# Optimization experiments

Hardware: AMD Instinct MI355X
Metric: run time of the kernel (lower is better)

## Reference

```python
import jax, jax.numpy as jnp
import numpy as np

N = 50000        # nodes
E = 800000       # random edges (self loops appended inside reference, per PyG default)
IN = 128         # in_channels
H1, C1 = 8, 64   # conv1: heads, hidden_channels
NUM_CLASSES = 2  # conv2 out (heads=1, concat=False)
NEG_SLOPE = 0.2  # PyG GATConv default LeakyReLU slope


def setup_inputs() -> dict:
    key = jax.random.key(0)
    ks = jax.random.split(key, 12)
    x = jax.random.normal(ks[0], (N, IN), dtype=jnp.float32)
    edge_index = jax.random.randint(ks[1], (2, E), 0, N)
    # conv1 params: W1 [IN, H1*C1], att vectors [H1, C1], bias [H1*C1]
    W1 = jax.random.normal(ks[2], (IN, H1 * C1), dtype=jnp.float32) / np.sqrt(IN)
    a_src1 = jax.random.normal(ks[3], (H1, C1), dtype=jnp.float32) / np.sqrt(C1)
    a_dst1 = jax.random.normal(ks[4], (H1, C1), dtype=jnp.float32) / np.sqrt(C1)
    b1 = jnp.zeros((H1 * C1,), dtype=jnp.float32)
    # conv2 params: heads=1, out=NUM_CLASSES
    W2 = jax.random.normal(ks[5], (H1 * C1, 1 * NUM_CLASSES), dtype=jnp.float32) / np.sqrt(H1 * C1)
    a_src2 = jax.random.normal(ks[6], (1, NUM_CLASSES), dtype=jnp.float32) / np.sqrt(NUM_CLASSES)
    a_dst2 = jax.random.normal(ks[7], (1, NUM_CLASSES), dtype=jnp.float32) / np.sqrt(NUM_CLASSES)
    b2 = jnp.zeros((NUM_CLASSES,), dtype=jnp.float32)
    return {"x": x, "edge_index": edge_index, "W1": W1, "a_src1": a_src1,
            "a_dst1": a_dst1, "b1": b1, "W2": W2, "a_src2": a_src2,
            "a_dst2": a_dst2, "b2": b2}


def gat_layer(x, src, dst, W, a_src, a_dst, bias, concat):
    n = x.shape[0]
    heads, ch = a_src.shape
    h = (x @ W).reshape(n, heads, ch)                      # [N,H,C]
    alpha_s = jnp.einsum('nhc,hc->nh', h, a_src)           # per-node src score
    alpha_d = jnp.einsum('nhc,hc->nh', h, a_dst)           # per-node dst score
    e = jax.nn.leaky_relu(alpha_s[src] + alpha_d[dst], NEG_SLOPE)  # [Etot,H]
    # segment softmax over edges grouped by destination node
    m = jax.ops.segment_max(e, dst, num_segments=n)
    ex = jnp.exp(e - m[dst])
    den = jax.ops.segment_sum(ex, dst, num_segments=n)
    alpha = ex / den[dst]                                  # [Etot,H]
    out = jax.ops.segment_sum(h[src] * alpha[:, :, None], dst, num_segments=n)  # [N,H,C]
    out = out.reshape(n, heads * ch) if concat else out.mean(axis=1)
    return out + bias


def reference(x, edge_index, W1, a_src1, a_dst1, b1, W2, a_src2, a_dst2, b2):
    n = x.shape[0]
    loops = jnp.arange(n, dtype=edge_index.dtype)
    src = jnp.concatenate([edge_index[0], loops])   # PyG add_self_loops=True
    dst = jnp.concatenate([edge_index[1], loops])
    h = gat_layer(x, src, dst, W1, a_src1, a_dst1, b1, concat=True)   # [N, H1*C1]
    h = jax.nn.elu(h)
    # dropout is identity in eval mode
    out = gat_layer(h, src, dst, W2, a_src2, a_dst2, b2, concat=False)  # [N, 2]
    return out
```

## Files before the change

kernel.cpp:

```cpp
#include <hip/hip_runtime.h>
#include <hip/hip_bf16.h>

#define NEG 0.2f
#define BKT 64

typedef __attribute__((ext_vector_type(8))) short bf16x8;
typedef __attribute__((ext_vector_type(4))) float f32x4;

static __device__ __forceinline__ unsigned short f2bf(float f) {
    union { float f; unsigned u; } v; v.f = f;
    unsigned r = v.u + 0x7fff + ((v.u >> 16) & 1);
    return (unsigned short)(r >> 16);
}
static __device__ __forceinline__ float bf_lo(unsigned u) {
    return __uint_as_float(u << 16);
}
static __device__ __forceinline__ float bf_hi(unsigned u) {
    return __uint_as_float(u & 0xffff0000u);
}

__global__ void k_build(const int* __restrict__ ei, int* __restrict__ deg,
                        int* __restrict__ csr,
                        const float* __restrict__ x, const float* __restrict__ W1,
                        unsigned short* __restrict__ xb, unsigned short* __restrict__ wt,
                        int tot, int E_, int n, int xel, int xelp) {
    int gid = blockIdx.x * 256 + threadIdx.x;
    if (gid < tot) {
        int s, d;
        if (gid < E_) { s = ei[gid]; d = ei[E_ + gid]; } else { s = d = gid - E_; }
        int slot = atomicAdd(&deg[d], 1);
        if (slot < BKT) csr[(size_t)d * BKT + slot] = s;
        return;
    }
    int i = gid - tot;
    if (i < 65536) {
        int c = i >> 7, k = i & 127;
        wt[i] = f2bf(W1[k * 512 + c]);
        return;
    }
    int i4 = (i - 65536) * 4;
    if (i4 >= xelp) return;
    float4 v = (i4 < xel) ? *(const float4*)(x + i4) : make_float4(0, 0, 0, 0);
    ushort4 o;
    o.x = f2bf(v.x); o.y = f2bf(v.y); o.z = f2bf(v.z); o.w = f2bf(v.w);
    *(ushort4*)(xb + i4) = o;
}

__global__ __launch_bounds__(256) void k_gemm1(const unsigned short* __restrict__ xb,
                                               const unsigned short* __restrict__ w1t,
                                               const float* __restrict__ a_src,
                                               const float* __restrict__ a_dst,
                                               unsigned short* __restrict__ h1b,
                                               float* __restrict__ as1,
                                               float* __restrict__ ad1, int n) {
    __shared__ unsigned short stg[4][16][72];
    int tid = threadIdx.x;
    int wave = tid >> 6, lane = tid & 63;
    int l15 = lane & 15, q = lane >> 4;
    int j = blockIdx.y;
    int col0 = j * 64;
    int rowblk = blockIdx.x * 256 + wave * 64;

    bf16x8 bfr[4][4];
    #pragma unroll
    for (int kb = 0; kb < 4; kb++)
        #pragma unroll
        for (int t = 0; t < 4; t++)
            bfr[kb][t] = *(const bf16x8*)(w1t + (size_t)(col0 + t * 16 + l15) * 128
                                          + kb * 32 + q * 8);
    float asv[4], adv[4];
    #pragma unroll
    for (int t = 0; t < 4; t++) {
        asv[t] = a_src[j * 64 + t * 16 + l15];
        adv[t] = a_dst[j * 64 + t * 16 + l15];
    }

    #pragma unroll
    for (int st = 0; st < 4; st++) {
        int row0 = rowblk + st * 16;
        f32x4 acc[4] = {};
        const unsigned short* ap = xb + (size_t)(row0 + l15) * 128 + q * 8;
        #pragma unroll
        for (int kb = 0; kb < 4; kb++) {
            bf16x8 af = *(const bf16x8*)(ap + kb * 32);
            #pragma unroll
            for (int t = 0; t < 4; t++)
                acc[t] = __builtin_amdgcn_mfma_f32_16x16x32_bf16(af, bfr[kb][t], acc[t], 0, 0, 0);
        }
        #pragma unroll
        for (int t = 0; t < 4; t++)
            #pragma unroll
            for (int r = 0; r < 4; r++)
                stg[wave][q * 4 + r][t * 16 + l15] = f2bf(acc[t][r]);
        #pragma unroll
        for (int p = 0; p < 2; p++) {
            int lr = p * 8 + (lane >> 3);
            int row = row0 + lr;
            int cd = (lane & 7) * 8;
            uint4 vv = *(const uint4*)&stg[wave][lr][cd];
            if (row < n)
                *(uint4*)(h1b + (size_t)row * 512 + col0 + cd) = vv;
        }
        float ps[4], pd[4];
        #pragma unroll
        for (int r = 0; r < 4; r++) {
            ps[r] = acc[0][r] * asv[0] + acc[1][r] * asv[1]
                  + acc[2][r] * asv[2] + acc[3][r] * asv[3];
            pd[r] = acc[0][r] * adv[0] + acc[1][r] * adv[1]
                  + acc[2][r] * adv[2] + acc[3][r] * adv[3];
            #pragma unroll
            for (int off = 1; off < 16; off <<= 1) {
                ps[r] += __shfl_xor(ps[r], off, 64);
                pd[r] += __shfl_xor(pd[r], off, 64);
            }
        }
        if (l15 < 4) {
            int r = l15;
            float vps = ps[0], vpd = pd[0];
            if (r == 1) { vps = ps[1]; vpd = pd[1]; }
            if (r == 2) { vps = ps[2]; vpd = pd[2]; }
            if (r == 3) { vps = ps[3]; vpd = pd[3]; }
            int row = row0 + q * 4 + r;
            if (row < n) { as1[row * 8 + j] = vps; ad1[row * 8 + j] = vpd; }
        }
    }
}

__global__ __launch_bounds__(256) void k_agg1(const unsigned short* __restrict__ h1b,
                                              const float* __restrict__ as1,
                                              const float* __restrict__ ad1,
                                              const float* __restrict__ b1,
                                              const float* __restrict__ W2,
                                              const int* __restrict__ deg,
                                              const int* __restrict__ csr,
                                              float* __restrict__ h2, int n) {
    int lane = threadIdx.x & 63;
    int v = blockIdx.x * 4 + (threadIdx.x >> 6);
    if (v >= n) return;
    int head = lane >> 3, c = lane * 8;
    int dv = deg[v]; if (dv > BKT) dv = BKT;
    const int* cp = csr + (size_t)v * BKT;
    float adh = ad1[v * 8 + head];
    float s = 0.f;
    float acc[8] = {};
    int i = 0;
    for (; i + 4 <= dv; i += 4) {
        int u0 = cp[i], u1 = cp[i + 1], u2 = cp[i + 2], u3 = cp[i + 3];
        float ea = as1[u0 * 8 + head] + adh;
        float eb = as1[u1 * 8 + head] + adh;
        float ec = as1[u2 * 8 + head] + adh;
        float ed = as1[u3 * 8 + head] + adh;
        uint4 h0 = *(const uint4*)(h1b + (size_t)u0 * 512 + c);
        uint4 h1 = *(const uint4*)(h1b + (size_t)u1 * 512 + c);
        uint4 h2v = *(const uint4*)(h1b + (size_t)u2 * 512 + c);
        uint4 h3 = *(const uint4*)(h1b + (size_t)u3 * 512 + c);
        ea = (ea >= 0.f) ? ea : NEG * ea;
        eb = (eb >= 0.f) ? eb : NEG * eb;
        ec = (ec >= 0.f) ? ec : NEG * ec;
        ed = (ed >= 0.f) ? ed : NEG * ed;
        float w0 = __expf(ea), w1 = __expf(eb), w2 = __expf(ec), w3 = __expf(ed);
        s += (w0 + w1) + (w2 + w3);
        acc[0] = fmaf(w3, bf_lo(h3.x), fmaf(w2, bf_lo(h2v.x), fmaf(w1, bf_lo(h1.x), fmaf(w0, bf_lo(h0.x), acc[0]))));
        acc[1] = fmaf(w3, bf_hi(h3.x), fmaf(w2, bf_hi(h2v.x), fmaf(w1, bf_hi(h1.x), fmaf(w0, bf_hi(h0.x), acc[1]))));
        acc[2] = fmaf(w3, bf_lo(h3.y), fmaf(w2, bf_lo(h2v.y), fmaf(w1, bf_lo(h1.y), fmaf(w0, bf_lo(h0.y), acc[2]))));
        acc[3] = fmaf(w3, bf_hi(h3.y), fmaf(w2, bf_hi(h2v.y), fmaf(w1, bf_hi(h1.y), fmaf(w0, bf_hi(h0.y), acc[3]))));
        acc[4] = fmaf(w3, bf_lo(h3.z), fmaf(w2, bf_lo(h2v.z), fmaf(w1, bf_lo(h1.z), fmaf(w0, bf_lo(h0.z), acc[4]))));
        acc[5] = fmaf(w3, bf_hi(h3.z), fmaf(w2, bf_hi(h2v.z), fmaf(w1, bf_hi(h1.z), fmaf(w0, bf_hi(h0.z), acc[5]))));
        acc[6] = fmaf(w3, bf_lo(h3.w), fmaf(w2, bf_lo(h2v.w), fmaf(w1, bf_lo(h1.w), fmaf(w0, bf_lo(h0.w), acc[6]))));
        acc[7] = fmaf(w3, bf_hi(h3.w), fmaf(w2, bf_hi(h2v.w), fmaf(w1, bf_hi(h1.w), fmaf(w0, bf_hi(h0.w), acc[7]))));
    }
    for (; i < dv; i++) {
        int u = cp[i];
        float e = as1[u * 8 + head] + adh;
        e = (e >= 0.f) ? e : NEG * e;
        float w = __expf(e);
        s += w;
        uint4 hv = *(const uint4*)(h1b + (size_t)u * 512 + c);
        acc[0] = fmaf(w, bf_lo(hv.x), acc[0]);
        acc[1] = fmaf(w, bf_hi(hv.x), acc[1]);
        acc[2] = fmaf(w, bf_lo(hv.y), acc[2]);
        acc[3] = fmaf(w, bf_hi(hv.y), acc[3]);
        acc[4] = fmaf(w, bf_lo(hv.z), acc[4]);
        acc[5] = fmaf(w, bf_hi(hv.z), acc[5]);
        acc[6] = fmaf(w, bf_lo(hv.w), acc[6]);
        acc[7] = fmaf(w, bf_hi(hv.w), acc[7]);
    }
    float inv = 1.0f / s;
    float4 ba = *(const float4*)(b1 + c);
    float4 bb = *(const float4*)(b1 + c + 4);
    float o[8] = {acc[0] * inv + ba.x, acc[1] * inv + ba.y,
                  acc[2] * inv + ba.z, acc[3] * inv + ba.w,
                  acc[4] * inv + bb.x, acc[5] * inv + bb.y,
                  acc[6] * inv + bb.z, acc[7] * inv + bb.w};
    #pragma unroll
    for (int jj = 0; jj < 8; jj++)
        o[jj] = (o[jj] > 0.f) ? o[jj] : (__expf(o[jj]) - 1.0f);
    const float4* wp = (const float4*)(W2 + c * 2);
    float4 w0 = wp[0], w1 = wp[1], w2 = wp[2], w3 = wp[3];
    float p0 = o[0] * w0.x + o[1] * w0.z + o[2] * w1.x + o[3] * w1.z
             + o[4] * w2.x + o[5] * w2.z + o[6] * w3.x + o[7] * w3.z;
    float p1 = o[0] * w0.y + o[1] * w0.w + o[2] * w1.y + o[3] * w1.w
             + o[4] * w2.y + o[5] * w2.w + o[6] * w3.y + o[7] * w3.w;
    #pragma unroll
    for (int off = 1; off < 64; off <<= 1) {
        p0 += __shfl_xor(p0, off, 64);
        p1 += __shfl_xor(p1, off, 64);
    }
    if (lane == 0) {
        h2[2 * v] = p0;
        h2[2 * v + 1] = p1;
    }
}

__global__ __launch_bounds__(256) void k_agg2(const float* __restrict__ h2,
                                              const float* __restrict__ a_src2,
                                              const float* __restrict__ a_dst2,
                                              const float* __restrict__ b2,
                                              const int* __restrict__ deg,
                                              const int* __restrict__ csr,
                                              float* __restrict__ out, int n) {
    int tid = threadIdx.x;
    int lane = tid & 63, wave = tid >> 6;
    int sub = lane & 7, g = lane >> 3;
    int v = blockIdx.x * 32 + wave * 8 + g;
    if (v >= n) return;
    int dv = deg[v]; if (dv > BKT) dv = BKT;
    const int* cp = csr + (size_t)v * BKT;
    float sa0 = a_src2[0], sa1 = a_src2[1];
    float da0 = a_dst2[0], da1 = a_dst2[1];
    float2 hv = *(const float2*)(h2 + 2 * v);
    float adv = hv.x * da0 + hv.y * da1;
    float s = 0.f, a0 = 0.f, a1 = 0.f;
    for (int i = sub; i < dv; i += 8) {
        int u = cp[i];
        float2 hu = *(const float2*)(h2 + 2 * u);
        float e = hu.x * sa0 + hu.y * sa1 + adv;
        e = (e >= 0.f) ? e : NEG * e;
        float w = __expf(e);
        s += w;
        a0 = fmaf(w, hu.x, a0);
        a1 = fmaf(w, hu.y, a1);
    }
    #pragma unroll
    for (int off = 1; off < 8; off <<= 1) {
        s  += __shfl_xor(s, off, 64);
        a0 += __shfl_xor(a0, off, 64);
        a1 += __shfl_xor(a1, off, 64);
    }
    if (sub == 0) {
        float inv = 1.0f / s;
        out[2 * v]     = a0 * inv + b2[0];
        out[2 * v + 1] = a1 * inv + b2[1];
    }
}

extern "C" void kernel_launch(void* const* d_in, const int* in_sizes, int n_in,
                              void* d_out, int out_size, void* d_ws, size_t ws_size,
                              hipStream_t stream) {
    const float* x      = (const float*)d_in[0];
    const int*   ei     = (const int*)d_in[1];
    const float* W1     = (const float*)d_in[2];
    const float* a_src1 = (const float*)d_in[3];
    const float* a_dst1 = (const float*)d_in[4];
    const float* b1     = (const float*)d_in[5];
    const float* W2     = (const float*)d_in[6];
    const float* a_src2 = (const float*)d_in[7];
    const float* a_dst2 = (const float*)d_in[8];
    const float* b2     = (const float*)d_in[9];
    float* out = (float*)d_out;

    int n  = in_sizes[0] / 128;
    int E_ = in_sizes[1] / 2;
    int tot = E_ + n;
    int rblk = (n + 255) / 256;
    int npad = rblk * 256;

    char* w = (char*)d_ws;
    auto alloc = [&](size_t bytes) {
        char* p = w; w += (bytes + 255) & ~(size_t)255; return p;
    };
    int*            deg    = (int*)alloc((size_t)n * 4);
    int*            csr    = (int*)alloc((size_t)n * BKT * 4);
    unsigned short* xb     = (unsigned short*)alloc((size_t)npad * 128 * 2);
    unsigned short* w1t    = (unsigned short*)alloc((size_t)512 * 128 * 2);
    unsigned short* h1b    = (unsigned short*)alloc((size_t)npad * 512 * 2);
    float*          as1    = (float*)alloc((size_t)n * 8 * 4);
    float*          ad1    = (float*)alloc((size_t)n * 8 * 4);
    float*          h2     = (float*)alloc((size_t)n * 2 * 4);

    int xel = n * 128, xelp = npad * 128;

    hipMemsetAsync(deg, 0, (size_t)n * 4, stream);

    int work = tot + 65536 + xelp / 4;
    k_build<<<(work + 255) / 256, 256, 0, stream>>>(ei, deg, csr, x, W1, xb, w1t,
                                                    tot, E_, n, xel, xelp);

    dim3 g1(rblk, 8);
    k_gemm1<<<g1, 256, 0, stream>>>(xb, w1t, a_src1, a_dst1, h1b, as1, ad1, n);

    int nb = (n + 3) / 4;
    k_agg1<<<nb, 256, 0, stream>>>(h1b, as1, ad1, b1, W2, deg, csr, h2, n);

    int ab = (n + 31) / 32;
    k_agg2<<<ab, 256, 0, stream>>>(h2, a_src2, a_dst2, b2, deg, csr, out, n);
}
```

Measured before the change: 331.7 us.

## Fuse CSR build and layer-1 GEMM into one launch with in-kernel bf16 conversion

Merges the edge-bucketing kernel and the first-layer GEMM into a single launch: the first blocks do the MFMA GEMM and the trailing blocks do the atomic CSR fill. The GEMM now reads fp32 x and W1 directly and converts to bf16 in registers, removing the separate bf16 staging buffers for x and transposed W1. This drops one kernel launch and a full write and reread of converted x. In exchange each GEMM block loads W1 with strided scalar fp32 loads, and x is read as fp32 (twice the bytes) by all eight column-group blocks.

```diff
diff --git a/kernel.cpp b/kernel.cpp
--- a/kernel.cpp
+++ b/kernel.cpp
@@ -19,55 +19,46 @@
     return __uint_as_float(u & 0xffff0000u);
 }
 
-__global__ void k_build(const int* __restrict__ ei, int* __restrict__ deg,
-                        int* __restrict__ csr,
-                        const float* __restrict__ x, const float* __restrict__ W1,
-                        unsigned short* __restrict__ xb, unsigned short* __restrict__ wt,
-                        int tot, int E_, int n, int xel, int xelp) {
-    int gid = blockIdx.x * 256 + threadIdx.x;
-    if (gid < tot) {
+__global__ __launch_bounds__(256) void k_big(const int* __restrict__ ei,
+                                             int* __restrict__ deg,
+                                             int* __restrict__ csr,
+                                             const float* __restrict__ x,
+                                             const float* __restrict__ W1,
+                                             const float* __restrict__ a_src,
+                                             const float* __restrict__ a_dst,
+                                             unsigned short* __restrict__ h1b,
+                                             float* __restrict__ as1,
+                                             float* __restrict__ ad1,
+                                             int E_, int n, int gblocks) {
+    int tid = threadIdx.x;
+    if ((int)blockIdx.x >= gblocks) {
+        int e = (blockIdx.x - gblocks) * 256 + tid;
+        int tot = E_ + n;
+        if (e >= tot) return;
         int s, d;
-        if (gid < E_) { s = ei[gid]; d = ei[E_ + gid]; } else { s = d = gid - E_; }
+        if (e < E_) { s = ei[e]; d = ei[E_ + e]; } else { s = d = e - E_; }
         int slot = atomicAdd(&deg[d], 1);
         if (slot < BKT) csr[(size_t)d * BKT + slot] = s;
         return;
     }
-    int i = gid - tot;
-    if (i < 65536) {
-        int c = i >> 7, k = i & 127;
-        wt[i] = f2bf(W1[k * 512 + c]);
-        return;
-    }
-    int i4 = (i - 65536) * 4;
-    if (i4 >= xelp) return;
-    float4 v = (i4 < xel) ? *(const float4*)(x + i4) : make_float4(0, 0, 0, 0);
-    ushort4 o;
-    o.x = f2bf(v.x); o.y = f2bf(v.y); o.z = f2bf(v.z); o.w = f2bf(v.w);
-    *(ushort4*)(xb + i4) = o;
-}
-
-__global__ __launch_bounds__(256) void k_gemm1(const unsigned short* __restrict__ xb,
-                                               const unsigned short* __restrict__ w1t,
-                                               const float* __restrict__ a_src,
-                                               const float* __restrict__ a_dst,
-                                               unsigned short* __restrict__ h1b,
-                                               float* __restrict__ as1,
-                                               float* __restrict__ ad1, int n) {
     __shared__ unsigned short stg[4][16][72];
-    int tid = threadIdx.x;
+    int g = blockIdx.x;
+    int j = g & 7, rb = g >> 3;
     int wave = tid >> 6, lane = tid & 63;
     int l15 = lane & 15, q = lane >> 4;
-    int j = blockIdx.y;
     int col0 = j * 64;
-    int rowblk = blockIdx.x * 256 + wave * 64;
+    int rowblk = rb * 256 + wave * 64;
 
     bf16x8 bfr[4][4];
     #pragma unroll
     for (int kb = 0; kb < 4; kb++)
         #pragma unroll
-        for (int t = 0; t < 4; t++)
-            bfr[kb][t] = *(const bf16x8*)(w1t + (size_t)(col0 + t * 16 + l15) * 128
-                                          + kb * 32 + q * 8);
+        for (int t = 0; t < 4; t++) {
+            const float* wp = W1 + (size_t)(kb * 32 + q * 8) * 512 + col0 + t * 16 + l15;
+            #pragma unroll
+            for (int e = 0; e < 8; e++)
+                bfr[kb][t][e] = (short)f2bf(wp[(size_t)e * 512]);
+        }
     float asv[4], adv[4];
     #pragma unroll
     for (int t = 0; t < 4; t++) {
@@ -78,11 +69,18 @@
     #pragma unroll
     for (int st = 0; st < 4; st++) {
         int row0 = rowblk + st * 16;
+        int ar = row0 + l15; if (ar > n - 1) ar = n - 1;
         f32x4 acc[4] = {};
-        const unsigned short* ap = xb + (size_t)(row0 + l15) * 128 + q * 8;
+        const float* ap = x + (size_t)ar * 128 + q * 8;
         #pragma unroll
         for (int kb = 0; kb < 4; kb++) {
-            bf16x8 af = *(const bf16x8*)(ap + kb * 32);
+            float4 v0 = *(const float4*)(ap + kb * 32);
+            float4 v1 = *(const float4*)(ap + kb * 32 + 4);
+            bf16x8 af;
+            af[0] = (short)f2bf(v0.x); af[1] = (short)f2bf(v0.y);
+            af[2] = (short)f2bf(v0.z); af[3] = (short)f2bf(v0.w);
+            af[4] = (short)f2bf(v1.x); af[5] = (short)f2bf(v1.y);
+            af[6] = (short)f2bf(v1.z); af[7] = (short)f2bf(v1.w);
             #pragma unroll
             for (int t = 0; t < 4; t++)
                 acc[t] = __builtin_amdgcn_mfma_f32_16x16x32_bf16(af, bfr[kb][t], acc[t], 0, 0, 0);
@@ -281,23 +279,18 @@
     };
     int*            deg    = (int*)alloc((size_t)n * 4);
     int*            csr    = (int*)alloc((size_t)n * BKT * 4);
-    unsigned short* xb     = (unsigned short*)alloc((size_t)npad * 128 * 2);
-    unsigned short* w1t    = (unsigned short*)alloc((size_t)512 * 128 * 2);
     unsigned short* h1b    = (unsigned short*)alloc((size_t)npad * 512 * 2);
     float*          as1    = (float*)alloc((size_t)n * 8 * 4);
     float*          ad1    = (float*)alloc((size_t)n * 8 * 4);
     float*          h2     = (float*)alloc((size_t)n * 2 * 4);
 
-    int xel = n * 128, xelp = npad * 128;
-
     hipMemsetAsync(deg, 0, (size_t)n * 4, stream);
 
-    int work = tot + 65536 + xelp / 4;
-    k_build<<<(work + 255) / 256, 256, 0, stream>>>(ei, deg, csr, x, W1, xb, w1t,
-                                                    tot, E_, n, xel, xelp);
-
-    dim3 g1(rblk, 8);
-    k_gemm1<<<g1, 256, 0, stream>>>(xb, w1t, a_src1, a_dst1, h1b, as1, ad1, n);
+    int gblocks = rblk * 8;
+    int sblocks = (tot + 255) / 256;
+    k_big<<<gblocks + sblocks, 256, 0, stream>>>(ei, deg, csr, x, W1,
+                                                 a_src1, a_dst1, h1b, as1, ad1,
+                                                 E_, n, gblocks);
 
     int nb = (n + 3) / 4;
     k_agg1<<<nb, 256, 0, stream>>>(h1b, as1, ad1, b1, W2, deg, csr, h2, n);
```

Result: faster. 313.9 us (-5.4%).
